# Performance work log

Measured on AMD Instinct MI355X. Metric: run time of the kernel, lower is better.

The kernel has to match this reference:

```python
import jax, jax.numpy as jnp
import numpy as np
from jax import lax

N, CI, CO, K, H, W_SP, M = 32, 256, 256, 3, 64, 64, 4
TAU = 1.0 / 30.0
PAD = 1  # spatial-preserving for k=3, stride=1, dilation=1


def setup_inputs() -> dict:
    key = jax.random.key(0)
    ks = jax.random.split(key, 6)
    # kaiming_normal fan_out for the kernel bank: fan_out = CO*K*K (per torch semantics on this 6D tensor layout)
    fan_out = CO * K * K
    std = np.sqrt(2.0 / fan_out)
    x = jax.random.normal(ks[0], (N, CI, H, W_SP), dtype=jnp.float32)
    Wbank = jax.random.normal(ks[1], (CO, M, CI, K, K), dtype=jnp.float32) * std
    Bbank = jnp.zeros((CO, M), dtype=jnp.float32)
    hid = CI // M  # att_fc hidden = in_channels // num_weights
    w1 = jax.random.normal(ks[2], (hid, CI), dtype=jnp.float32) * np.sqrt(1.0 / CI)
    b1 = jnp.zeros((hid,), dtype=jnp.float32)
    w2 = jax.random.normal(ks[3], (M, hid), dtype=jnp.float32) * np.sqrt(1.0 / hid)
    b2 = jnp.zeros((M,), dtype=jnp.float32)
    return {"x": x, "Wbank": Wbank, "Bbank": Bbank, "w1": w1, "b1": b1, "w2": w2, "b2": b2}


def reference(x, Wbank, Bbank, w1, b1, w2, b2):
    n, ci, h, w = x.shape
    co = Wbank.shape[0]
    # attention over kernels: global avg pool -> 1x1 conv MLP -> softmax(logits * tau)
    pooled = jnp.mean(x, axis=(2, 3))                      # N,Ci
    hmid = jax.nn.relu(pooled @ w1.T + b1)                 # N,hid
    logits = hmid @ w2.T + b2                              # N,M
    pi = jax.nn.softmax(logits * TAU, axis=1)              # N,M
    # per-sample aggregated kernels and biases
    wn = jnp.einsum("nm,omikl->noikl", pi, Wbank)          # N,Co,Ci,K,K
    bn = pi @ Bbank.T                                      # N,Co
    # batch-as-groups conv2d (spatial-preserving)
    xg = x.reshape(1, n * ci, h, w)
    wg = wn.reshape(n * co, ci, K, K)
    y = lax.conv_general_dilated(
        xg, wg,
        window_strides=(1, 1),
        padding=[(PAD, PAD), (PAD, PAD)],
        rhs_dilation=(1, 1),
        dimension_numbers=("NCHW", "OIHW", "NCHW"),
        feature_group_count=n,
    )
    y = y.reshape(n, co, h, w) + bn[:, :, None, None]
    return y
```

## Files before the change

### kernel.cpp

```cpp
#include <hip/hip_runtime.h>
#include <hip/hip_bf16.h>
#include <stdint.h>

typedef __bf16 bf16;
typedef __bf16 bf16x8 __attribute__((ext_vector_type(8)));
typedef float f32x4 __attribute__((ext_vector_type(4)));

#define TAU (1.0f/30.0f)

#define NB 32
#define CI 256
#define CO 256
#define HH 64
#define WW 64
#define HID 64

#define WN_ELEMS ((size_t)NB*8*9*16*512)
#define WN_BYTES (WN_ELEMS*2)
#define XB_ELEMS ((size_t)NB*32*64*64*8)
#define XB_BYTES (XB_ELEMS*2)

__device__ __forceinline__ void async16(void* lds_uniform_base, const void* g_perlane) {
  __builtin_amdgcn_global_load_lds(
      (const __attribute__((address_space(1))) uint32_t*)g_perlane,
      (__attribute__((address_space(3))) uint32_t*)lds_uniform_base, 16, 0, 0);
}

__global__ void cvt_pool_kernel(const float* __restrict__ x, bf16* __restrict__ xb,
                                float* __restrict__ pooled) {
  const int cg = blockIdx.x, n = blockIdx.y, tid = threadIdx.x;
  const float* base = x + ((size_t)n*CI + cg*8)*4096;
  bf16* ob = xb + ((size_t)n*32 + cg)*4096*8;
  float s[8];
#pragma unroll
  for (int j = 0; j < 8; ++j) s[j] = 0.f;
  for (int it = 0; it < 16; ++it) {
    int pos = it*256 + tid;
    bf16x8 o;
#pragma unroll
    for (int j = 0; j < 8; ++j) {
      float v = base[(size_t)j*4096 + pos];
      s[j] += v;
      o[j] = (bf16)v;
    }
    *(bf16x8*)(ob + (size_t)pos*8) = o;
  }
  __shared__ float red[4][8];
#pragma unroll
  for (int j = 0; j < 8; ++j)
#pragma unroll
    for (int off = 32; off; off >>= 1) s[j] += __shfl_xor(s[j], off);
  int wv = tid >> 6, lane = tid & 63;
  if (lane == 0)
#pragma unroll
    for (int j = 0; j < 8; ++j) red[wv][j] = s[j];
  __syncthreads();
  if (tid < 8) {
    float t = red[0][tid] + red[1][tid] + red[2][tid] + red[3][tid];
    pooled[n*CI + cg*8 + tid] = t * (1.0f/4096.0f);
  }
}

__global__ void attn_kernel(const float* __restrict__ pooled,
                            const float* __restrict__ w1, const float* __restrict__ b1,
                            const float* __restrict__ w2, const float* __restrict__ b2,
                            float* __restrict__ pi) {
  int n = blockIdx.x, h = threadIdx.x;
  __shared__ float hm[HID];
  __shared__ float lgs[4];
  const float* pr = pooled + n*CI;
  float s = b1[h];
  for (int c = 0; c < CI; ++c) s += pr[c] * w1[h*CI + c];
  hm[h] = s > 0.f ? s : 0.f;
  __syncthreads();
  if (h < 4) {
    float lg = b2[h];
    for (int k = 0; k < HID; ++k) lg += hm[k] * w2[h*HID + k];
    lgs[h] = lg * TAU;
  }
  __syncthreads();
  if (h == 0) {
    float mx = fmaxf(fmaxf(lgs[0], lgs[1]), fmaxf(lgs[2], lgs[3]));
    float e0 = expf(lgs[0]-mx), e1 = expf(lgs[1]-mx), e2 = expf(lgs[2]-mx), e3 = expf(lgs[3]-mx);
    float inv = 1.f / (e0+e1+e2+e3);
    pi[n*4+0] = e0*inv; pi[n*4+1] = e1*inv; pi[n*4+2] = e2*inv; pi[n*4+3] = e3*inv;
  }
}

__global__ void agg_kernel(const float* __restrict__ Wbank, const float* __restrict__ pi,
                           bf16* __restrict__ wn) {
  int wid = blockIdx.x * 4 + (threadIdx.x >> 6);
  int lane = threadIdx.x & 63;
  int c = wid / 144;
  int rem = wid - c*144;
  int kk = rem >> 4;
  int cbg = rem & 15;
  int co  = cbg*16 + (lane & 15);
  int ci0 = c*32 + (lane >> 4)*8;
  float w[4][8];
#pragma unroll
  for (int m = 0; m < 4; ++m)
#pragma unroll
    for (int j = 0; j < 8; ++j)
      w[m][j] = Wbank[(size_t)((co*4 + m)*256 + ci0 + j)*9 + kk];
  for (int n = 0; n < NB; ++n) {
    float p0 = pi[n*4+0], p1 = pi[n*4+1], p2 = pi[n*4+2], p3 = pi[n*4+3];
    bf16x8 o;
#pragma unroll
    for (int j = 0; j < 8; ++j)
      o[j] = (bf16)(p0*w[0][j] + p1*w[1][j] + p2*w[2][j] + p3*w[3][j]);
    *(bf16x8*)(wn + ((size_t)n*1152 + c*144 + kk*16 + cbg)*512 + lane*8) = o;
  }
}

#define XROWS 10
#define XW 66
#define XS_E (4*XROWS*XW*8)
#define WA_E (9*4*512)

__global__ __launch_bounds__(256, 2)
void conv_kernel(const bf16* __restrict__ xb, const bf16* __restrict__ wn,
                 const float* __restrict__ pi, const float* __restrict__ Bbank,
                 float* __restrict__ y) {
  __shared__ __align__(16) bf16 xs[XS_E];
  __shared__ __align__(16) bf16 wa[WA_E];
  __shared__ float bns[64];
  const int tid = threadIdx.x;
  const int wv = tid >> 6, lane = tid & 63;
  const int l = lane & 15, u = lane >> 4;
  const int flat = blockIdx.x;
  const int wid = ((flat & 7) << 7) + (flat >> 3);
  const int n   = wid >> 5;
  const int hwb = (wid >> 2) & 7;
  const int cot = wid & 3;
  const int h0 = hwb * 8;

  const bf16* wnb = wn + (size_t)n*1152*512 + (size_t)(cot*4 + wv)*512 + lane*8;
  const bf16* xgb = xb + (size_t)n*32*4096*8 + lane*8;

  bf16x8 wstg[9];
  auto LOADW = [&](int c) {
    const bf16* seg = wnb + (size_t)c*144*512;
#pragma unroll
    for (int kk = 0; kk < 9; ++kk)
      wstg[kk] = *(const bf16x8*)(seg + (size_t)kk*16*512);
  };

  LOADW(0);

  for (int i = tid; i < XS_E/8; i += 256) ((int4*)xs)[i] = int4{0,0,0,0};
  if (tid < 64) {
    int co = cot*64 + tid;
    bns[tid] = pi[n*4+0]*Bbank[co*4+0] + pi[n*4+1]*Bbank[co*4+1]
             + pi[n*4+2]*Bbank[co*4+2] + pi[n*4+3]*Bbank[co*4+3];
  }

  f32x4 acc[2][4][4];
#pragma unroll
  for (int o = 0; o < 2; ++o)
#pragma unroll
    for (int a = 0; a < 4; ++a)
#pragma unroll
      for (int b = 0; b < 4; ++b)
#pragma unroll
        for (int k = 0; k < 4; ++k) acc[o][a][b][k] = 0.f;

  for (int c = 0; c < 8; ++c) {
    __syncthreads();
    {
      const bf16* xg = xgb + (size_t)(c*4 + wv)*4096*8;
#pragma unroll
      for (int r = 0; r < XROWS; ++r) {
        int hp = h0 - 1 + r;
        if (hp >= 0 && hp < HH)
          async16(&xs[((wv*XROWS + r)*XW + 1)*8], xg + (size_t)hp*64*8);
      }
    }
#pragma unroll
    for (int kk = 0; kk < 9; ++kk)
      *(int4*)(&wa[kk*2048 + wv*512 + lane*8]) = *(int4*)&wstg[kk];
    __syncthreads();
    if (c < 7) LOADW(c + 1);

    auto LD = [&](int rr, int f, int kx) {
      return *(const bf16x8*)(&xs[((u*XROWS + wv*2 + rr)*XW + f*16 + l + kx)*8]);
    };
    auto MM = [&](int ky, int kx, bf16x8 (&lo)[4], bf16x8 (&hi)[4]) {
      const int kk = ky*3 + kx;
      __builtin_amdgcn_s_setprio(1);
#pragma unroll
      for (int cb = 0; cb < 4; ++cb) {
        bf16x8 afr = *(const bf16x8*)(&wa[kk*2048 + cb*512 + lane*8]);
#pragma unroll
        for (int f = 0; f < 4; ++f) {
          acc[0][cb][f] = __builtin_amdgcn_mfma_f32_16x16x32_bf16(afr, lo[f], acc[0][cb][f], 0, 0, 0);
          acc[1][cb][f] = __builtin_amdgcn_mfma_f32_16x16x32_bf16(afr, hi[f], acc[1][cb][f], 0, 0, 0);
        }
      }
      __builtin_amdgcn_s_setprio(0);
    };
#pragma unroll
    for (int kx = 0; kx < 3; ++kx) {
      bf16x8 rA[4], rB[4];
#pragma unroll
      for (int f = 0; f < 4; ++f) { rA[f] = LD(0, f, kx); rB[f] = LD(1, f, kx); }
      MM(0, kx, rA, rB);
#pragma unroll
      for (int f = 0; f < 4; ++f) rA[f] = LD(2, f, kx);
      MM(1, kx, rB, rA);
#pragma unroll
      for (int f = 0; f < 4; ++f) rB[f] = LD(3, f, kx);
      MM(2, kx, rA, rB);
    }
  }
#pragma unroll
  for (int o = 0; o < 2; ++o) {
    const int h = h0 + wv*2 + o;
#pragma unroll
    for (int cb = 0; cb < 4; ++cb) {
#pragma unroll
      for (int f = 0; f < 4; ++f) {
        const int wcol = f*16 + l;
#pragma unroll
        for (int r4 = 0; r4 < 4; ++r4) {
          const int col = cb*16 + u*4 + r4;
          y[(((size_t)n*CO + cot*64 + col)*HH + h)*WW + wcol] = acc[o][cb][f][r4] + bns[col];
        }
      }
    }
  }
}

extern "C" void kernel_launch(void* const* d_in, const int* in_sizes, int n_in,
                              void* d_out, int out_size, void* d_ws, size_t ws_size,
                              hipStream_t stream) {
  const float* x     = (const float*)d_in[0];
  const float* Wbank = (const float*)d_in[1];
  const float* Bbank = (const float*)d_in[2];
  const float* w1    = (const float*)d_in[3];
  const float* b1    = (const float*)d_in[4];
  const float* w2    = (const float*)d_in[5];
  const float* b2    = (const float*)d_in[6];
  float* y = (float*)d_out;

  bf16*  wn     = (bf16*)d_ws;
  bf16*  xb     = (bf16*)((char*)d_ws + WN_BYTES);
  float* pooled = (float*)((char*)d_ws + WN_BYTES + XB_BYTES);
  float* pi     = pooled + NB*CI;

  dim3 cg(32, NB);
  cvt_pool_kernel<<<cg, 256, 0, stream>>>(x, xb, pooled);
  attn_kernel<<<NB, HID, 0, stream>>>(pooled, w1, b1, w2, b2, pi);
  agg_kernel<<<288, 256, 0, stream>>>(Wbank, pi, wn);
  conv_kernel<<<1024, 256, 0, stream>>>(xb, wn, pi, Bbank, y);
}
```

Baseline: 189.2 us.

## Stream conv weights directly into registers with a 3-slot rotating prefetch, dropping LDS staging

Removes the LDS weight buffer and the per-chunk register-to-LDS copy, so each wave loads the A fragments for all four output-channel blocks straight from global memory into registers. A three-slot ring prefetches the tap two steps ahead and runs into the next input-channel chunk, hiding load latency behind the MFMAs. This cuts LDS footprint and LDS traffic, but each wave now fetches 4x the weight data from global/L2 (redundant across waves), and the extra live registers may pressure occupancy.

```diff
diff --git a/kernel.cpp b/kernel.cpp
--- a/kernel.cpp
+++ b/kernel.cpp
@@ -116,14 +116,12 @@
 #define XROWS 10
 #define XW 66
 #define XS_E (4*XROWS*XW*8)
-#define WA_E (9*4*512)
 
 __global__ __launch_bounds__(256, 2)
 void conv_kernel(const bf16* __restrict__ xb, const bf16* __restrict__ wn,
                  const float* __restrict__ pi, const float* __restrict__ Bbank,
                  float* __restrict__ y) {
   __shared__ __align__(16) bf16 xs[XS_E];
-  __shared__ __align__(16) bf16 wa[WA_E];
   __shared__ float bns[64];
   const int tid = threadIdx.x;
   const int wv = tid >> 6, lane = tid & 63;
@@ -135,18 +133,18 @@
   const int cot = wid & 3;
   const int h0 = hwb * 8;
 
-  const bf16* wnb = wn + (size_t)n*1152*512 + (size_t)(cot*4 + wv)*512 + lane*8;
-  const bf16* xgb = xb + (size_t)n*32*4096*8 + lane*8;
-
-  bf16x8 wstg[9];
-  auto LOADW = [&](int c) {
-    const bf16* seg = wnb + (size_t)c*144*512;
-#pragma unroll
-    for (int kk = 0; kk < 9; ++kk)
-      wstg[kk] = *(const bf16x8*)(seg + (size_t)kk*16*512);
+  const bf16* wbase = wn + (size_t)n*1152*512 + (size_t)cot*4*512 + lane*8;
+  const bf16* xgb   = xb + (size_t)n*32*4096*8 + lane*8;
+
+  bf16x8 P[3][4];
+  auto LOADT = [&](int cc, int kk, int slot) {
+#pragma unroll
+    for (int cb = 0; cb < 4; ++cb)
+      P[slot][cb] = *(const bf16x8*)(wbase + ((size_t)cc*144 + (size_t)kk*16 + cb)*512);
   };
 
-  LOADW(0);
+  LOADT(0, 0, 0);
+  LOADT(0, 3, 1);
 
   for (int i = tid; i < XS_E/8; i += 256) ((int4*)xs)[i] = int4{0,0,0,0};
   if (tid < 64) {
@@ -165,6 +163,9 @@
 #pragma unroll
         for (int k = 0; k < 4; ++k) acc[o][a][b][k] = 0.f;
 
+  const int lk_kk[9]   = {6, 1, 4, 7, 2, 5, 8, 0, 3};
+  const int lk_slot[9] = {2, 0, 1, 2, 0, 1, 2, 0, 1};
+
   for (int c = 0; c < 8; ++c) {
     __syncthreads();
     {
@@ -176,21 +177,17 @@
           async16(&xs[((wv*XROWS + r)*XW + 1)*8], xg + (size_t)hp*64*8);
       }
     }
-#pragma unroll
-    for (int kk = 0; kk < 9; ++kk)
-      *(int4*)(&wa[kk*2048 + wv*512 + lane*8]) = *(int4*)&wstg[kk];
     __syncthreads();
-    if (c < 7) LOADW(c + 1);
+    const int cnx = (c < 7) ? c + 1 : 7;
 
     auto LD = [&](int rr, int f, int kx) {
       return *(const bf16x8*)(&xs[((u*XROWS + wv*2 + rr)*XW + f*16 + l + kx)*8]);
     };
-    auto MM = [&](int ky, int kx, bf16x8 (&lo)[4], bf16x8 (&hi)[4]) {
-      const int kk = ky*3 + kx;
+    auto MMp = [&](int slot, bf16x8 (&lo)[4], bf16x8 (&hi)[4]) {
       __builtin_amdgcn_s_setprio(1);
 #pragma unroll
       for (int cb = 0; cb < 4; ++cb) {
-        bf16x8 afr = *(const bf16x8*)(&wa[kk*2048 + cb*512 + lane*8]);
+        bf16x8 afr = P[slot][cb];
 #pragma unroll
         for (int f = 0; f < 4; ++f) {
           acc[0][cb][f] = __builtin_amdgcn_mfma_f32_16x16x32_bf16(afr, lo[f], acc[0][cb][f], 0, 0, 0);
@@ -199,18 +196,19 @@
       }
       __builtin_amdgcn_s_setprio(0);
     };
+
 #pragma unroll
     for (int kx = 0; kx < 3; ++kx) {
       bf16x8 rA[4], rB[4];
 #pragma unroll
       for (int f = 0; f < 4; ++f) { rA[f] = LD(0, f, kx); rB[f] = LD(1, f, kx); }
-      MM(0, kx, rA, rB);
+      { const int s = kx*3 + 0; LOADT(s >= 7 ? cnx : c, lk_kk[s], lk_slot[s]); MMp(s % 3, rA, rB); }
 #pragma unroll
       for (int f = 0; f < 4; ++f) rA[f] = LD(2, f, kx);
-      MM(1, kx, rB, rA);
+      { const int s = kx*3 + 1; LOADT(s >= 7 ? cnx : c, lk_kk[s], lk_slot[s]); MMp(s % 3, rB, rA); }
 #pragma unroll
       for (int f = 0; f < 4; ++f) rB[f] = LD(3, f, kx);
-      MM(2, kx, rA, rB);
+      { const int s = kx*3 + 2; LOADT(s >= 7 ? cnx : c, lk_kk[s], lk_slot[s]); MMp(s % 3, rA, rB); }
     }
   }
 #pragma unroll
```

After: 415.6 us. 120% more time.
